# Kernel optimization log

Hardware: AMD Instinct MI355X
Metric: run time of the kernel (lower is better)

## Reference

```python
import jax, jax.numpy as jnp
import numpy as np
from jax import lax

INT8_NARROW = (-127.0, 127.0)   # brevitas Int8WeightPerTensorFloat (narrow range)
INT8_FULL = (-128.0, 127.0)     # brevitas Int8ActPerTensorFloat
INT32 = (-2.0**31, 2.0**31 - 1)


def _fake_quant(v, scale, qmin, qmax):
    # round-to-nearest, clip, dequant (per-tensor)
    return jnp.clip(jnp.round(v / scale), qmin, qmax) * scale


def _conv(x, w, stride):
    return lax.conv_general_dilated(
        x, w, window_strides=(stride, stride), padding=[(1, 1), (1, 1)],
        dimension_numbers=("NCHW", "OIHW", "NCHW"))


def setup_inputs() -> dict:
    key = jax.random.key(0)
    ks = jax.random.split(key, 5)
    B, Cin, Cout, H = 64, 256, 512, 28
    x = jax.random.normal(ks[0], (B, Cin, H, H), dtype=jnp.float32)
    w1 = jax.random.normal(ks[1], (Cout, Cin, 3, 3), dtype=jnp.float32) * 0.05
    b1 = jax.random.normal(ks[2], (Cout,), dtype=jnp.float32) * 0.01
    w2 = jax.random.normal(ks[3], (Cout, Cout, 3, 3), dtype=jnp.float32) * 0.05
    b2 = jax.random.normal(ks[4], (Cout,), dtype=jnp.float32) * 0.01
    return {
        "x": x, "w1": w1, "b1": b1, "w2": w2, "b2": b2,
        "in_scale": jnp.full((1,), 0.05, dtype=jnp.float32),
        "act1_scale": jnp.full((1,), 0.05, dtype=jnp.float32),
        "act2_scale": jnp.full((1,), 0.05, dtype=jnp.float32),
    }


def reference(x, w1, b1, w2, b2, in_scale, act1_scale, act2_scale):
    s_in = in_scale[0]
    s_a1 = act1_scale[0]
    s_a2 = act2_scale[0]

    # conv1: per-tensor int8 weight fake-quant (max-abs stats, narrow range)
    s_w1 = jnp.max(jnp.abs(w1)) / 127.0
    wq1 = _fake_quant(w1, s_w1, *INT8_NARROW)
    bq1 = _fake_quant(b1, s_in * s_w1, *INT32)  # Int32Bias: scale = in_scale*w_scale
    out = _conv(x, wq1, 2) + bq1[None, :, None, None]

    # act1: int8 activation fake-quant (learned per-tensor scale)
    out = _fake_quant(out, s_a1, *INT8_FULL)

    # conv2
    s_w2 = jnp.max(jnp.abs(w2)) / 127.0
    wq2 = _fake_quant(w2, s_w2, *INT8_NARROW)
    bq2 = _fake_quant(b2, s_a1 * s_w2, *INT32)
    out = _conv(out, wq2, 1) + bq2[None, :, None, None]

    # act2
    out = _fake_quant(out, s_a2, *INT8_FULL)
    return out
```

## Files before the change

kernel.cpp:

```cpp
#include <hip/hip_runtime.h>

typedef int i32x4 __attribute__((ext_vector_type(4)));

__device__ __forceinline__ void gl_lds16(const signed char* g, signed char* l) {
    __builtin_amdgcn_global_load_lds(
        (const __attribute__((address_space(1))) void*)g,
        (__attribute__((address_space(3))) void*)l, 16, 0, 0);
}

#define XQ_SCALE 2048.0f
#define XQ_DELTA (1.0f / 2048.0f)

__device__ __forceinline__ float block_max256(const float* __restrict__ part, int base,
                                              float* __restrict__ sred) {
    float m = part[base + (threadIdx.x & 255)];
#pragma unroll
    for (int off = 32; off > 0; off >>= 1)
        m = fmaxf(m, __shfl_down(m, off));
    __syncthreads();
    if ((threadIdx.x & 63) == 0) sred[threadIdx.x >> 6] = m;
    __syncthreads();
    return fmaxf(fmaxf(sred[0], sred[1]), fmaxf(sred[2], sred[3]));
}

__global__ __launch_bounds__(256) void fused_pre_kernel(
    const float* __restrict__ x,
    const float* __restrict__ w1, const float* __restrict__ w2,
    float* __restrict__ part,
    signed char* __restrict__ xhi, signed char* __restrict__ xlo,
    signed char* __restrict__ act) {
    __shared__ float t[128][33];
    __shared__ float sred[4];
    const int blk = blockIdx.x;
    const int tid = threadIdx.x;
    const uint4 z = {0, 0, 0, 0};

    if (blk < 512) {
        const bool second = blk >= 256;
        const float* w = second ? w2 : w1;
        const int n4 = second ? 589824 : 294912;
        float m = 0.0f;
        for (int i = (blk & 255) * 256 + tid; i < n4; i += 65536) {
            float4 v = ((const float4*)w)[i];
            m = fmaxf(m, fmaxf(fmaxf(fabsf(v.x), fabsf(v.y)), fmaxf(fabsf(v.z), fabsf(v.w))));
        }
#pragma unroll
        for (int off = 32; off > 0; off >>= 1)
            m = fmaxf(m, __shfl_down(m, off));
        if ((tid & 63) == 0) sred[tid >> 6] = m;
        __syncthreads();
        if (tid == 0)
            part[blk] = fmaxf(fmaxf(sred[0], sred[1]), fmaxf(sred[2], sred[3]));
    } else if (blk < 976) {
        const int thr = (blk - 512) * 256 + tid;
        const int b = thr / (116 * 16);
        const int rr = thr - b * (116 * 16);
        const int p = rr >> 4;
        const int ch = rr & 15;
        int h, w;
        if (p < 30)      { h = 0;          w = p; }
        else if (p < 60) { h = 29;         w = p - 30; }
        else if (p < 88) { h = p - 60 + 1; w = 0; }
        else             { h = p - 88 + 1; w = 29; }
        const int off = (b * 900 + h * 30 + w) * 256 + ch * 16;
        *(uint4*)(xhi + off) = z;
        *(uint4*)(xlo + off) = z;
    } else if (blk < 1456) {
        const int thr = (blk - 976) * 256 + tid;
        const int b = thr / (60 * 32);
        const int rr = thr - b * (60 * 32);
        const int p = rr >> 5;
        const int ch = rr & 31;
        int h, w;
        if (p < 16)      { h = 0;          w = p; }
        else if (p < 32) { h = 15;         w = p - 16; }
        else if (p < 46) { h = p - 32 + 1; w = 0; }
        else             { h = p - 46 + 1; w = 15; }
        const int off = (b * 256 + h * 16 + w) * 512 + ch * 16;
        *(uint4*)(act + off) = z;
    } else {
        const int xb = blk - 1456;
        const int hwb = xb % 25;
        const int rest = xb / 25;
        const int cb = rest & 1;
        const int b = rest >> 1;
        const int c0 = cb * 128;
        const int hw0 = hwb * 32;
#pragma unroll
        for (int ci = 0; ci < 16; ++ci) {
            const int crow = (tid >> 5) + ci * 8;
            const int hw = hw0 + (tid & 31);
            float v = 0.0f;
            if (hw < 784) v = x[(b * 256 + c0 + crow) * 784 + hw];
            t[crow][tid & 31] = v;
        }
        __syncthreads();
        const int hw_l = tid >> 3;
        const int cg = (tid & 7) * 16;
        const int hw = hw0 + hw_l;
        if (hw < 784) {
            union { signed char c[16]; uint4 u; } ph, pl;
#pragma unroll
            for (int j = 0; j < 16; ++j) {
                const float v = t[cg + j][hw_l];
                int q = (int)rintf(v * XQ_SCALE);
                q = max(-16383, min(16383, q));
                ph.c[j] = (signed char)(q >> 7);
                pl.c[j] = (signed char)(q & 127);
            }
            const int r = hw / 28;
            const int o = (b * 900 + (r + 1) * 30 + (hw - r * 28) + 1) * 256 + c0 + cg;
            *(uint4*)&xhi[o] = ph.u;
            *(uint4*)&xlo[o] = pl.u;
        }
    }
}

__global__ __launch_bounds__(256) void prep_w_kernel(
    const float* __restrict__ w1, const float* __restrict__ w2,
    const float* __restrict__ b1, const float* __restrict__ b2,
    const float* __restrict__ part,
    const float* __restrict__ in_scale, const float* __restrict__ act1_scale,
    signed char* __restrict__ wq1, signed char* __restrict__ wq2,
    float* __restrict__ bq1, float* __restrict__ bq2,
    float* __restrict__ wmax) {
    __shared__ __align__(16) signed char sw[4608];
    __shared__ float sred[4];
    const int blk = blockIdx.x;
    const int tid = threadIdx.x;

    if (blk < 512) {
        const float inv_s = 127.0f / block_max256(part, 0, sred);
        const int n = blk;
#pragma unroll
        for (int rd = 0; rd < 9; ++rd) {
            const int idx = rd * 256 + tid;
            const float v = w1[n * 2304 + idx];
            float q = rintf(v * inv_s);
            q = fminf(fmaxf(q, -127.0f), 127.0f);
            const int cin = idx / 9;
            const int r = idx - cin * 9;
            sw[r * 256 + cin] = (signed char)(int)q;
        }
        __syncthreads();
        if (tid < 144) *(uint4*)&wq1[n * 2304 + tid * 16] = *(const uint4*)&sw[tid * 16];
    } else if (blk < 1024) {
        const float inv_s = 127.0f / block_max256(part, 256, sred);
        const int n = blk - 512;
#pragma unroll
        for (int rd = 0; rd < 18; ++rd) {
            const int idx = rd * 256 + tid;
            const float v = w2[n * 4608 + idx];
            float q = rintf(v * inv_s);
            q = fminf(fmaxf(q, -127.0f), 127.0f);
            const int cin = idx / 9;
            const int r = idx - cin * 9;
            sw[r * 512 + cin] = (signed char)(int)q;
        }
        __syncthreads();
        for (int o = tid; o < 288; o += 256)
            *(uint4*)&wq2[n * 4608 + o * 16] = *(const uint4*)&sw[o * 16];
    } else {
        const float m1 = block_max256(part, 0, sred);
        const float m2 = block_max256(part, 256, sred);
        if (tid == 0) { wmax[0] = m1; wmax[1] = m2; }
        for (int idx = tid; idx < 1024; idx += 256) {
            if (idx < 512) {
                const float s = (*in_scale) * (m1 * (1.0f / 127.0f));
                float q = rintf(b1[idx] / s);
                q = fminf(fmaxf(q, -2147483648.0f), 2147483648.0f);
                bq1[idx] = q * s;
            } else {
                const int j = idx - 512;
                const float s = (*act1_scale) * (m2 * (1.0f / 127.0f));
                float q = rintf(b2[j] / s);
                q = fminf(fmaxf(q, -2147483648.0f), 2147483648.0f);
                bq2[j] = q * s;
            }
        }
    }
}

template<int CIN, int STRIDE, int HP, int HOUT, bool SPLIT, bool FINAL>
__global__ __launch_bounds__(256, SPLIT ? 2 : 3) void conv_gemm_kernel(
    const signed char* __restrict__ Ahi,
    const signed char* __restrict__ Alo,
    const signed char* __restrict__ Wt,
    const float* __restrict__ bias,
    const float* __restrict__ wmax,
    const float* __restrict__ s_pre,
    const float* __restrict__ s_act,
    signed char* __restrict__ act_out,
    float* __restrict__ out_final)
{
    constexpr int K = 9 * CIN;
    constexpr int HW = HOUT * HOUT;
    constexpr int NIT = K / 128;
    constexpr int NC = SPLIT ? 8 : 6;
    constexpr int BUFSZ = SPLIT ? 32768 : 24576;
    constexpr int NB = SPLIT ? 4 : 2;

    __shared__ __align__(16) signed char smem[2 * BUFSZ];

    const int tid = threadIdx.x;
    const int lane = tid & 63;
    const int wv = tid >> 6;
    const int pair = wv >> 1;
    const int nh = wv & 1;
    const int quad = lane >> 4;
    const int l16 = lane & 15;
    const int m0 = blockIdx.y * 64;
    const int n0 = blockIdx.x * 128;

    const int lrow = lane >> 3;
    const int koff = ((lane & 7) ^ lrow) * 16;

    const signed char* srcb[NC];
    int dsto[NC];
    bool isA[NC];
    if constexpr (SPLIT) {
#pragma unroll
        for (int i = 0; i < NC; ++i) {
            const int g = wv * 8 + i;
            const int type = g >> 3;
            if (type >= 2) {
                const int c = g - 16;
                srcb[i] = Wt + (n0 + c * 8 + lrow) * K + koff;
                dsto[i] = 16384 + c * 1024;
                isA[i] = false;
            } else {
                const int c = g & 7;
                const int m = m0 + c * 8 + lrow;
                const int b = m / HW;
                const int rem = m - b * HW;
                const int oh = rem / HOUT;
                const int ow = rem - oh * HOUT;
                const int off = ((b * HP + oh * STRIDE) * HP + ow * STRIDE) * CIN + koff;
                srcb[i] = (type == 0 ? Ahi : Alo) + off;
                dsto[i] = type * 8192 + c * 1024;
                isA[i] = true;
            }
        }
    } else {
#pragma unroll
        for (int i = 0; i < NC; ++i) {
            const int g = wv * 6 + i;
            if (g < 8) {
                const int c = g;
                const int m = m0 + c * 8 + lrow;
                const int b = m / HW;
                const int rem = m - b * HW;
                const int oh = rem / HOUT;
                const int ow = rem - oh * HOUT;
                const int off = ((b * HP + oh * STRIDE) * HP + ow * STRIDE) * CIN + koff;
                srcb[i] = Ahi + off;
                dsto[i] = c * 1024;
                isA[i] = true;
            } else {
                const int c = g - 8;
                srcb[i] = Wt + (n0 + c * 8 + lrow) * K + koff;
                dsto[i] = 8192 + c * 1024;
                isA[i] = false;
            }
        }
    }

    const int aoff0 = SPLIT ? (pair * 8192) : 0;
    const int boff0 = SPLIT ? 16384 : 8192;
    const int nfix  = SPLIT ? (nh * 64) : (wv * 32);

    i32x4 acc[4][NB];
#pragma unroll
    for (int mi = 0; mi < 4; ++mi)
#pragma unroll
        for (int ni = 0; ni < NB; ++ni)
            acc[mi][ni] = i32x4{0, 0, 0, 0};

    auto STAGE = [&](int bo, int it) {
        const int k0 = it * 128;
        const int r9 = k0 / CIN;
        const int kh = r9 / 3;
        const int kw = r9 - kh * 3;
        const int ashift = (kh * HP + kw) * CIN + (k0 & (CIN - 1));
#pragma unroll
        for (int i = 0; i < NC; ++i)
            gl_lds16(srcb[i] + (isA[i] ? ashift : k0), &smem[bo + dsto[i]]);
    };

    auto COMPUTE = [&](int bo) {
#pragma unroll
        for (int ks = 0; ks < 2; ++ks) {
            i32x4 af[4], bfr[NB];
#pragma unroll
            for (int mi = 0; mi < 4; ++mi) {
                const int row = mi * 16 + l16;
                const int sl = ((ks * 4 + quad) ^ (row & 7)) * 16;
                af[mi] = *(const i32x4*)&smem[bo + aoff0 + row * 128 + sl];
            }
#pragma unroll
            for (int ni = 0; ni < NB; ++ni) {
                const int row = nfix + ni * 16 + l16;
                const int sl = ((ks * 4 + quad) ^ (row & 7)) * 16;
                bfr[ni] = *(const i32x4*)&smem[bo + boff0 + row * 128 + sl];
            }
#pragma unroll
            for (int mi = 0; mi < 4; ++mi)
#pragma unroll
                for (int ni = 0; ni < NB; ++ni)
                    acc[mi][ni] = __builtin_amdgcn_mfma_i32_16x16x64_i8(af[mi], bfr[ni], acc[mi][ni], 0, 0, 0);
        }
    };

    STAGE(0, 0);
    __syncthreads();
    for (int it = 0; it < NIT; it += 2) {
        if (it + 1 < NIT) STAGE(BUFSZ, it + 1);
        COMPUTE(0);
        __syncthreads();
        if (it + 2 < NIT) STAGE(0, it + 2);
        COMPUTE(BUFSZ);
        __syncthreads();
    }

    if constexpr (SPLIT) {
        if (pair == 1) {
#pragma unroll
            for (int mi = 0; mi < 4; ++mi)
#pragma unroll
                for (int ni = 0; ni < 4; ++ni)
                    *(i32x4*)&smem[nh * 16384 + (mi * 4 + ni) * 1024 + lane * 16] = acc[mi][ni];
        }
        __syncthreads();
        if (pair == 1) return;
#pragma unroll
        for (int mi = 0; mi < 4; ++mi)
#pragma unroll
            for (int ni = 0; ni < 4; ++ni) {
                const i32x4 other = *(const i32x4*)&smem[nh * 16384 + (mi * 4 + ni) * 1024 + lane * 16];
                acc[mi][ni] = acc[mi][ni] * 128 + other;
            }
    }

    float alpha = (*wmax) * (1.0f / 127.0f);
    if (FINAL) alpha *= *s_pre;
    if (SPLIT) alpha *= XQ_DELTA;
    const float sact = *s_act;

    float bv[NB];
#pragma unroll
    for (int ni = 0; ni < NB; ++ni)
        bv[ni] = bias[n0 + nfix + ni * 16 + l16];

#pragma unroll
    for (int mi = 0; mi < 4; ++mi) {
#pragma unroll
        for (int i = 0; i < 4; ++i) {
            const int m = m0 + mi * 16 + quad * 4 + i;
            const int b = m / HW;
            const int rem = m - b * HW;
            const int oh = rem / HOUT;
            const int ow = rem - oh * HOUT;
#pragma unroll
            for (int ni = 0; ni < NB; ++ni) {
                const int col = n0 + nfix + ni * 16 + l16;
                const float v = (float)acc[mi][ni][i] * alpha + bv[ni];
                float q = rintf(v / sact);
                q = fminf(fmaxf(q, -128.0f), 127.0f);
                if (FINAL) {
                    out_final[(b * 512 + col) * HW + oh * HOUT + ow] = q * sact;
                } else {
                    act_out[(b * 256 + (oh + 1) * 16 + (ow + 1)) * 512 + col] = (signed char)(int)q;
                }
            }
        }
    }
}

extern "C" void kernel_launch(void* const* d_in, const int* in_sizes, int n_in,
                              void* d_out, int out_size, void* d_ws, size_t ws_size,
                              hipStream_t stream) {
    const float* x  = (const float*)d_in[0];
    const float* w1 = (const float*)d_in[1];
    const float* b1 = (const float*)d_in[2];
    const float* w2 = (const float*)d_in[3];
    const float* b2 = (const float*)d_in[4];
    const float* in_scale   = (const float*)d_in[5];
    const float* act1_scale = (const float*)d_in[6];
    const float* act2_scale = (const float*)d_in[7];
    float* out = (float*)d_out;

    char* ws = (char*)d_ws;
    float* part = (float*)(ws + 0);
    float* wmax = (float*)(ws + 2048);
    float* bq1 = (float*)(ws + 2176);
    float* bq2 = (float*)(ws + 4224);
    signed char* wq1 = (signed char*)(ws + 8192);
    signed char* wq2 = (signed char*)(ws + 1187840);
    signed char* xhi = (signed char*)(ws + 3547136);
    signed char* xlo = (signed char*)(ws + 18292736);
    signed char* act = (signed char*)(ws + 33038336);

    fused_pre_kernel<<<4656, 256, 0, stream>>>(x, w1, w2, part, xhi, xlo, act);

    prep_w_kernel<<<1025, 256, 0, stream>>>(w1, w2, b1, b2, part, in_scale, act1_scale,
                                            wq1, wq2, bq1, bq2, wmax);

    conv_gemm_kernel<256, 2, 30, 14, true, false><<<dim3(4, 196), 256, 0, stream>>>(
        xhi, xlo, wq1, bq1, wmax, act1_scale, act1_scale, act, nullptr);

    conv_gemm_kernel<512, 1, 16, 14, false, true><<<dim3(4, 196), 256, 0, stream>>>(
        act, nullptr, wq2, bq2, wmax + 1, act1_scale, act2_scale, nullptr, out);
}
```

Baseline: 243.9 us.

## Restructure int8 GEMM main loop to overlap global loads with MFMAs via explicit waitcnts

The double-buffered main loop now loads all LDS fragments for a stage into registers first. It then issues the next global->LDS prefetch into the freed buffer and runs the MFMAs afterwards at raised wave priority. Full __syncthreads are replaced with fine-grained vmcnt/lgkmcnt waits, raw s_barrier and sched_barrier, so that two stages of global loads stay in flight. This adds register pressure and relies on hand-counted vmcnt values matching the number of outstanding loads per stage.

After: 234.1 us. -4.0%, faster.

```diff
diff --git a/kernel.cpp b/kernel.cpp
--- a/kernel.cpp
+++ b/kernel.cpp
@@ -6,6 +6,13 @@
     __builtin_amdgcn_global_load_lds(
         (const __attribute__((address_space(1))) void*)g,
         (__attribute__((address_space(3))) void*)l, 16, 0, 0);
+}
+
+__device__ __forceinline__ i32x4 lds_read_b128(const signed char* p) {
+    i32x4 r;
+    const unsigned a = (unsigned)(uintptr_t)(const __attribute__((address_space(3))) signed char*)p;
+    asm volatile("ds_read_b128 %0, %1" : "=v"(r) : "v"(a));
+    return r;
 }
 
 #define XQ_SCALE 2048.0f
@@ -287,42 +294,88 @@
             gl_lds16(srcb[i] + (isA[i] ? ashift : k0), &smem[bo + dsto[i]]);
     };
 
-    auto COMPUTE = [&](int bo) {
+    auto LOADFRAGS = [&](int bo, i32x4 (&af)[2][4], i32x4 (&bf)[2][NB]) {
 #pragma unroll
         for (int ks = 0; ks < 2; ++ks) {
-            i32x4 af[4], bfr[NB];
 #pragma unroll
             for (int mi = 0; mi < 4; ++mi) {
                 const int row = mi * 16 + l16;
                 const int sl = ((ks * 4 + quad) ^ (row & 7)) * 16;
-                af[mi] = *(const i32x4*)&smem[bo + aoff0 + row * 128 + sl];
+                af[ks][mi] = lds_read_b128(&smem[bo + aoff0 + row * 128 + sl]);
             }
 #pragma unroll
             for (int ni = 0; ni < NB; ++ni) {
                 const int row = nfix + ni * 16 + l16;
                 const int sl = ((ks * 4 + quad) ^ (row & 7)) * 16;
-                bfr[ni] = *(const i32x4*)&smem[bo + boff0 + row * 128 + sl];
-            }
+                bf[ks][ni] = lds_read_b128(&smem[bo + boff0 + row * 128 + sl]);
+            }
+        }
+    };
+
+    auto MFMAS = [&](i32x4 (&af)[2][4], i32x4 (&bf)[2][NB]) {
+        __builtin_amdgcn_s_setprio(1);
+#pragma unroll
+        for (int ks = 0; ks < 2; ++ks)
 #pragma unroll
             for (int mi = 0; mi < 4; ++mi)
 #pragma unroll
                 for (int ni = 0; ni < NB; ++ni)
-                    acc[mi][ni] = __builtin_amdgcn_mfma_i32_16x16x64_i8(af[mi], bfr[ni], acc[mi][ni], 0, 0, 0);
-        }
+                    acc[mi][ni] = __builtin_amdgcn_mfma_i32_16x16x64_i8(af[ks][mi], bf[ks][ni], acc[mi][ni], 0, 0, 0);
+        __builtin_amdgcn_s_setprio(0);
     };
 
+    auto WAIT_NC = [&]() {
+        if constexpr (SPLIT) asm volatile("s_waitcnt vmcnt(8)" ::: "memory");
+        else                 asm volatile("s_waitcnt vmcnt(6)" ::: "memory");
+    };
+
+    i32x4 af[2][4], bf[2][NB];
+
     STAGE(0, 0);
-    __syncthreads();
-    for (int it = 0; it < NIT; it += 2) {
-        if (it + 1 < NIT) STAGE(BUFSZ, it + 1);
-        COMPUTE(0);
-        __syncthreads();
-        if (it + 2 < NIT) STAGE(0, it + 2);
-        COMPUTE(BUFSZ);
-        __syncthreads();
-    }
+    STAGE(BUFSZ, 1);
+
+    for (int it = 0; it < NIT - 2; it += 2) {
+        WAIT_NC();
+        __builtin_amdgcn_s_barrier();
+        __builtin_amdgcn_sched_barrier(0);
+        LOADFRAGS(0, af, bf);
+        asm volatile("s_waitcnt lgkmcnt(0)" ::: "memory");
+        __builtin_amdgcn_sched_barrier(0);
+        __builtin_amdgcn_s_barrier();
+        __builtin_amdgcn_sched_barrier(0);
+        STAGE(0, it + 2);
+        MFMAS(af, bf);
+
+        WAIT_NC();
+        __builtin_amdgcn_s_barrier();
+        __builtin_amdgcn_sched_barrier(0);
+        LOADFRAGS(BUFSZ, af, bf);
+        asm volatile("s_waitcnt lgkmcnt(0)" ::: "memory");
+        __builtin_amdgcn_sched_barrier(0);
+        __builtin_amdgcn_s_barrier();
+        __builtin_amdgcn_sched_barrier(0);
+        if (it + 3 < NIT) STAGE(BUFSZ, it + 3);
+        MFMAS(af, bf);
+    }
+
+    WAIT_NC();
+    __builtin_amdgcn_s_barrier();
+    __builtin_amdgcn_sched_barrier(0);
+    LOADFRAGS(0, af, bf);
+    asm volatile("s_waitcnt lgkmcnt(0)" ::: "memory");
+    __builtin_amdgcn_sched_barrier(0);
+    MFMAS(af, bf);
+
+    asm volatile("s_waitcnt vmcnt(0)" ::: "memory");
+    __builtin_amdgcn_s_barrier();
+    __builtin_amdgcn_sched_barrier(0);
+    LOADFRAGS(BUFSZ, af, bf);
+    asm volatile("s_waitcnt lgkmcnt(0)" ::: "memory");
+    __builtin_amdgcn_sched_barrier(0);
+    MFMAS(af, bf);
 
     if constexpr (SPLIT) {
+        __syncthreads();
         if (pair == 1) {
 #pragma unroll
             for (int mi = 0; mi < 4; ++mi)
```

## Load weight fragments directly to registers and hand-schedule LDS pipeline with waitcnts

Applied to the files above, without the earlier changes.

The B (weight) operand is no longer staged through LDS. Each wave loads its weight fragments straight from global memory into registers with double-buffered global_load_dwordx4, which shrinks the LDS buffers so only the activation tiles pass through shared memory. The main loop becomes a hand-scheduled window using explicit vmcnt/lgkmcnt waits, raw s_barrier, sched_barriers and setprio around the MFMA groups, so fragment reads and next-stage prefetches overlap with matrix math. This removes the LDS traffic and bank pressure for B, at the cost of more VGPRs, uncoalesced per-lane global reads of weights, and fragile inline-asm wait counts.

Result: slower. 306.9 us (+25.8%).

```diff
diff --git a/kernel.cpp b/kernel.cpp
--- a/kernel.cpp
+++ b/kernel.cpp
@@ -6,6 +6,17 @@
     __builtin_amdgcn_global_load_lds(
         (const __attribute__((address_space(1))) void*)g,
         (__attribute__((address_space(3))) void*)l, 16, 0, 0);
+}
+
+__device__ __forceinline__ i32x4 lds_read_b128(const signed char* p) {
+    i32x4 r;
+    const unsigned a = (unsigned)(uintptr_t)(const __attribute__((address_space(3))) signed char*)p;
+    asm volatile("ds_read_b128 %0, %1" : "=v"(r) : "v"(a));
+    return r;
+}
+
+__device__ __forceinline__ void glb_b128(const signed char* p, i32x4& dst) {
+    asm volatile("global_load_dwordx4 %0, %1, off" : "=v"(dst) : "v"(p));
 }
 
 #define XQ_SCALE 2048.0f
@@ -196,9 +207,9 @@
     constexpr int K = 9 * CIN;
     constexpr int HW = HOUT * HOUT;
     constexpr int NIT = K / 128;
-    constexpr int NC = SPLIT ? 8 : 6;
-    constexpr int BUFSZ = SPLIT ? 32768 : 24576;
+    constexpr int ACH = SPLIT ? 4 : 2;
     constexpr int NB = SPLIT ? 4 : 2;
+    constexpr int BUFSZ = SPLIT ? 16384 : 8192;
 
     __shared__ __align__(16) signed char smem[2 * BUFSZ];
 
@@ -215,59 +226,36 @@
     const int lrow = lane >> 3;
     const int koff = ((lane & 7) ^ lrow) * 16;
 
-    const signed char* srcb[NC];
-    int dsto[NC];
-    bool isA[NC];
-    if constexpr (SPLIT) {
-#pragma unroll
-        for (int i = 0; i < NC; ++i) {
-            const int g = wv * 8 + i;
-            const int type = g >> 3;
-            if (type >= 2) {
-                const int c = g - 16;
-                srcb[i] = Wt + (n0 + c * 8 + lrow) * K + koff;
-                dsto[i] = 16384 + c * 1024;
-                isA[i] = false;
-            } else {
-                const int c = g & 7;
-                const int m = m0 + c * 8 + lrow;
-                const int b = m / HW;
-                const int rem = m - b * HW;
-                const int oh = rem / HOUT;
-                const int ow = rem - oh * HOUT;
-                const int off = ((b * HP + oh * STRIDE) * HP + ow * STRIDE) * CIN + koff;
-                srcb[i] = (type == 0 ? Ahi : Alo) + off;
-                dsto[i] = type * 8192 + c * 1024;
-                isA[i] = true;
-            }
-        }
-    } else {
-#pragma unroll
-        for (int i = 0; i < NC; ++i) {
-            const int g = wv * 6 + i;
-            if (g < 8) {
-                const int c = g;
-                const int m = m0 + c * 8 + lrow;
-                const int b = m / HW;
-                const int rem = m - b * HW;
-                const int oh = rem / HOUT;
-                const int ow = rem - oh * HOUT;
-                const int off = ((b * HP + oh * STRIDE) * HP + ow * STRIDE) * CIN + koff;
-                srcb[i] = Ahi + off;
-                dsto[i] = c * 1024;
-                isA[i] = true;
-            } else {
-                const int c = g - 8;
-                srcb[i] = Wt + (n0 + c * 8 + lrow) * K + koff;
-                dsto[i] = 8192 + c * 1024;
-                isA[i] = false;
-            }
-        }
-    }
-
     const int aoff0 = SPLIT ? (pair * 8192) : 0;
-    const int boff0 = SPLIT ? 16384 : 8192;
     const int nfix  = SPLIT ? (nh * 64) : (wv * 32);
+
+    const signed char* srcb[ACH];
+    int dsto[ACH];
+#pragma unroll
+    for (int i = 0; i < ACH; ++i) {
+        int limb, c;
+        if constexpr (SPLIT) {
+            const int g = wv * 4 + i;
+            limb = g >> 3;
+            c = g & 7;
+        } else {
+            limb = 0;
+            c = wv * 2 + i;
+        }
+        const int m = m0 + c * 8 + lrow;
+        const int b = m / HW;
+        const int rem = m - b * HW;
+        const int oh = rem / HOUT;
+        const int ow = rem - oh * HOUT;
+        const int off = ((b * HP + oh * STRIDE) * HP + ow * STRIDE) * CIN + koff;
+        srcb[i] = (limb ? Alo : Ahi) + off;
+        dsto[i] = limb * 8192 + c * 1024;
+    }
+
+    const signed char* bptr[NB];
+#pragma unroll
+    for (int ni = 0; ni < NB; ++ni)
+        bptr[ni] = Wt + (n0 + nfix + ni * 16 + l16) * K + quad * 16;
 
     i32x4 acc[4][NB];
 #pragma unroll
@@ -275,6 +263,9 @@
 #pragma unroll
         for (int ni = 0; ni < NB; ++ni)
             acc[mi][ni] = i32x4{0, 0, 0, 0};
+
+    i32x4 af[2][4];
+    i32x4 bA[2][NB], bB[2][NB];
 
     auto STAGE = [&](int bo, int it) {
         const int k0 = it * 128;
@@ -283,46 +274,77 @@
         const int kw = r9 - kh * 3;
         const int ashift = (kh * HP + kw) * CIN + (k0 & (CIN - 1));
 #pragma unroll
-        for (int i = 0; i < NC; ++i)
-            gl_lds16(srcb[i] + (isA[i] ? ashift : k0), &smem[bo + dsto[i]]);
-    };
-
-    auto COMPUTE = [&](int bo) {
-#pragma unroll
-        for (int ks = 0; ks < 2; ++ks) {
-            i32x4 af[4], bfr[NB];
+        for (int i = 0; i < ACH; ++i)
+            gl_lds16(srcb[i] + ashift, &smem[bo + dsto[i]]);
+    };
+
+    auto BLOAD = [&](i32x4 (&dst)[2][NB], int it1) {
+        const int k0 = it1 * 128;
+#pragma unroll
+        for (int ks = 0; ks < 2; ++ks)
+#pragma unroll
+            for (int ni = 0; ni < NB; ++ni)
+                glb_b128(bptr[ni] + k0 + ks * 64, dst[ks][ni]);
+    };
+
+    auto LOADFRAGS = [&](int bo) {
+#pragma unroll
+        for (int ks = 0; ks < 2; ++ks)
 #pragma unroll
             for (int mi = 0; mi < 4; ++mi) {
                 const int row = mi * 16 + l16;
                 const int sl = ((ks * 4 + quad) ^ (row & 7)) * 16;
-                af[mi] = *(const i32x4*)&smem[bo + aoff0 + row * 128 + sl];
+                af[ks][mi] = lds_read_b128(&smem[bo + aoff0 + row * 128 + sl]);
             }
-#pragma unroll
-            for (int ni = 0; ni < NB; ++ni) {
-                const int row = nfix + ni * 16 + l16;
-                const int sl = ((ks * 4 + quad) ^ (row & 7)) * 16;
-                bfr[ni] = *(const i32x4*)&smem[bo + boff0 + row * 128 + sl];
-            }
-#pragma unroll
-            for (int mi = 0; mi < 4; ++mi)
-#pragma unroll
-                for (int ni = 0; ni < NB; ++ni)
-                    acc[mi][ni] = __builtin_amdgcn_mfma_i32_16x16x64_i8(af[mi], bfr[ni], acc[mi][ni], 0, 0, 0);
-        }
+    };
+
+    auto MFMAS_KS = [&](int ks, i32x4 (&bc)[2][NB]) {
+        __builtin_amdgcn_s_setprio(1);
+#pragma unroll
+        for (int mi = 0; mi < 4; ++mi)
+#pragma unroll
+            for (int ni = 0; ni < NB; ++ni)
+                acc[mi][ni] = __builtin_amdgcn_mfma_i32_16x16x64_i8(af[ks][mi], bc[ks][ni], acc[mi][ni], 0, 0, 0);
+        __builtin_amdgcn_s_setprio(0);
+    };
+
+    auto WAIT_ACH = [&]() {
+        if constexpr (SPLIT) asm volatile("s_waitcnt vmcnt(4)" ::: "memory");
+        else                 asm volatile("s_waitcnt vmcnt(2)" ::: "memory");
+    };
+
+    auto WINDOW = [&](int bo, int it, i32x4 (&bc)[2][NB], i32x4 (&bn)[2][NB],
+                      bool bload, bool stage, bool last) {
+        if (last) asm volatile("s_waitcnt vmcnt(0)" ::: "memory");
+        else      WAIT_ACH();
+        __builtin_amdgcn_s_barrier();
+        __builtin_amdgcn_sched_barrier(0);
+        LOADFRAGS(bo);
+        asm volatile("s_waitcnt lgkmcnt(4)" ::: "memory");
+        __builtin_amdgcn_sched_barrier(0);
+        MFMAS_KS(0, bc);
+        asm volatile("s_waitcnt lgkmcnt(0)" ::: "memory");
+        __builtin_amdgcn_sched_barrier(0);
+        __builtin_amdgcn_s_barrier();
+        __builtin_amdgcn_sched_barrier(0);
+        if (bload) BLOAD(bn, it + 1);
+        if (stage) STAGE(bo, it + 2);
+        MFMAS_KS(1, bc);
     };
 
     STAGE(0, 0);
-    __syncthreads();
-    for (int it = 0; it < NIT; it += 2) {
-        if (it + 1 < NIT) STAGE(BUFSZ, it + 1);
-        COMPUTE(0);
-        __syncthreads();
-        if (it + 2 < NIT) STAGE(0, it + 2);
-        COMPUTE(BUFSZ);
-        __syncthreads();
-    }
+    BLOAD(bA, 0);
+    STAGE(BUFSZ, 1);
+
+    for (int it = 0; it < NIT - 2; it += 2) {
+        WINDOW(0,     it,     bA, bB, true, true, false);
+        WINDOW(BUFSZ, it + 1, bB, bA, true, true, false);
+    }
+    WINDOW(0,     NIT - 2, bA, bB, true,  false, false);
+    WINDOW(BUFSZ, NIT - 1, bB, bA, false, false, true);
 
     if constexpr (SPLIT) {
+        __syncthreads();
         if (pair == 1) {
 #pragma unroll
             for (int mi = 0; mi < 4; ++mi)
```
